# Kernel tuning notes

Measured on AMD Instinct MI355X. Metric: run time of the kernel, lower is better.

## Reference

```python
import jax, jax.numpy as jnp
import numpy as np

VOCAB, EMBED, NFEAT, T, HIDDEN, NCLASS, BATCH = 50000, 50, 3, 120, 300, 5, 1024
D_IN = NFEAT * EMBED  # 150


def setup_inputs() -> dict:
    key = jax.random.key(0)
    ks = jax.random.split(key, 5)
    s_in = 1.0 / np.sqrt(D_IN)
    s_h = 1.0 / np.sqrt(HIDDEN)
    return {
        "ids": jax.random.randint(ks[0], (BATCH, T, NFEAT), 0, VOCAB, dtype=jnp.int32),
        "embed": jax.random.normal(ks[1], (VOCAB, EMBED), dtype=jnp.float32),
        "Wx": jax.random.normal(ks[2], (D_IN, 4 * HIDDEN), dtype=jnp.float32) * s_in,
        "Wh": jax.random.normal(ks[3], (HIDDEN, 4 * HIDDEN), dtype=jnp.float32) * s_h,
        "b": jnp.zeros((4 * HIDDEN,), dtype=jnp.float32),
        "U": jax.random.normal(ks[4], (HIDDEN, NCLASS), dtype=jnp.float32) * s_h,
        "b2": jnp.zeros((NCLASS,), dtype=jnp.float32),
    }


def reference(ids, embed, Wx, Wh, b, U, b2):
    # Embedding lookup + concat windows: (B, T, 3) -> (B, T, 150)
    x = embed[ids].reshape(ids.shape[0], T, D_IN)
    # Precompute input contribution for all timesteps: (B, T, 4H)
    xz = jnp.einsum("btd,dg->btg", x, Wx) + b
    xz = jnp.transpose(xz, (1, 0, 2))  # (T, B, 4H)

    def step(carry, xz_t):
        c, h = carry
        z = xz_t + h @ Wh  # (B, 4H)
        i, f, g, o = jnp.split(z, 4, axis=-1)
        i = jax.nn.sigmoid(i)
        f = jax.nn.sigmoid(f)
        o = jax.nn.sigmoid(o)
        g = jnp.tanh(g)
        c = f * c + i * g
        h = o * jnp.tanh(c)
        # dropout at inference (keep_prob=1) is identity
        y = h @ U + b2  # (B, C)
        return (c, h), y

    B = ids.shape[0]
    init = (jnp.zeros((B, HIDDEN), x.dtype), jnp.zeros((B, HIDDEN), x.dtype))
    _, ys = jax.lax.scan(step, init, xz)  # ys: (T, B, C)
    return jnp.transpose(ys, (1, 0, 2))  # (B, T, C)
```

## Files before the change

### kernel.cpp

```cpp
#include <hip/hip_runtime.h>


#define BATCH 1024
#define TT    120
#define HID   300
#define KX    160
#define KH    320
#define SL    64
#define HSL   60
#define NCOL  1280
#define GH    5
#define GB    32
#define BS    32
#define XST   168
#define FSTR  32
#define NSLOT 3
#define NB    256

typedef __attribute__((ext_vector_type(8))) short bf16x8;
typedef __attribute__((ext_vector_type(4))) float f32x4;

__device__ __forceinline__ unsigned short f2b(float f) {
  union { float f; unsigned u; } v; v.f = f;
  unsigned r = v.u + 0x7fffu + ((v.u >> 16) & 1u);
  return (unsigned short)(r >> 16);
}
__device__ __forceinline__ float sigm(float x) {
  return __builtin_amdgcn_rcpf(1.f + __expf(-x));
}
__device__ __forceinline__ float tanhf_(float x) {
  return 2.f * __builtin_amdgcn_rcpf(1.f + __expf(-2.f * x)) - 1.f;
}

__global__ void k_reorder_wh(const float* __restrict__ W, unsigned short* __restrict__ Wp) {
  int tid = blockIdx.x * 256 + threadIdx.x;
  if (tid >= KH * NCOL) return;
  int c = tid % NCOL, k = tid / NCOL;
  int js = k >> 6, v0 = k & 63;
  int j = c >> 8, r = c & 255, g = r >> 6, u0 = r & 63;
  float val = 0.f;
  if (v0 < HSL && u0 < HSL) val = W[(js * HSL + v0) * 1200 + g * 300 + j * HSL + u0];
  Wp[((k >> 3) * NCOL + c) * 8 + (k & 7)] = f2b(val);
}

__global__ void k_reorder_wx(const float* __restrict__ W, unsigned short* __restrict__ Wp) {
  int tid = blockIdx.x * 256 + threadIdx.x;
  if (tid >= KX * NCOL) return;
  int c = tid % NCOL, k = tid / NCOL;
  int j = c >> 8, r = c & 255, g = r >> 6, u0 = r & 63;
  float val = 0.f;
  if (k < 150 && u0 < HSL) val = W[k * 1200 + g * 300 + j * HSL + u0];
  Wp[((k >> 3) * NCOL + c) * 8 + (k & 7)] = f2b(val);
}

__global__ void k_reorder_b(const float* __restrict__ b, float* __restrict__ bp) {
  int c = blockIdx.x * 256 + threadIdx.x;
  if (c >= NCOL) return;
  int j = c >> 8, r = c & 255, g = r >> 6, u0 = r & 63;
  bp[c] = (u0 < HSL) ? b[g * 300 + j * HSL + u0] : 0.f;
}

__global__ void k_reorder_u(const float* __restrict__ U, unsigned short* __restrict__ Up) {
  int tid = blockIdx.x * 256 + threadIdx.x;
  if (tid >= KH * 16) return;
  int n = tid % 16, k = tid / 16;
  int js = k >> 6, v0 = k & 63;
  float v = (v0 < HSL && n < 5) ? U[(js * HSL + v0) * 5 + n] : 0.f;
  Up[((k >> 3) * 16 + n) * 8 + (k & 7)] = f2b(v);
}

__launch_bounds__(256, 1)
__global__ void k_lstm(const int* __restrict__ ids, const float* __restrict__ embed,
                       const unsigned short* __restrict__ Wp,
                       const unsigned short* __restrict__ Wxp,
                       const float* __restrict__ bp,
                       const unsigned short* __restrict__ Up,
                       unsigned short* __restrict__ hbuf,
                       int* __restrict__ flags,
                       int* __restrict__ xcd_cnt,
                       const float* __restrict__ b2,
                       float* __restrict__ out) {
  __shared__ __align__(16) unsigned short x_lds[2][BS * XST];
  __shared__ char lds_pad[61440];
  __shared__ int role[2];

  const int tid = threadIdx.x;
  if (tid == 0) {
    ((volatile char*)lds_pad)[0] = 0;
    int xcd = __builtin_amdgcn_s_getreg(63508) & 7;
    int rank = atomicAdd(&xcd_cnt[xcd], 1);
    role[0] = xcd; role[1] = rank;
  }
  __syncthreads();
  const int xcd = role[0], rank = role[1];
  if (rank >= GH * 4) return;
  const int bg = xcd * 4 + rank / GH;
  const int j  = rank % GH;

  const int lane = tid & 63, w = tid >> 6;
  const int l15 = lane & 15, l4 = lane >> 4;

  if (tid < BS) {
#pragma unroll
    for (int bq = 0; bq < 2; ++bq)
      for (int e = 150; e < XST; ++e) x_lds[bq][tid * XST + e] = 0;
  }

  const int colb = j * 256 + w * 16 + l15;

  bf16x8 bh[10][4], bx[5][4];
#pragma unroll
  for (int kk = 0; kk < 10; ++kk)
#pragma unroll
    for (int g = 0; g < 4; ++g)
      bh[kk][g] = *(const bf16x8*)(Wp + ((kk * 4 + l4) * NCOL + colb + g * 64) * 8);
#pragma unroll
  for (int kk = 0; kk < 5; ++kk)
#pragma unroll
    for (int g = 0; g < 4; ++g)
      bx[kk][g] = *(const bf16x8*)(Wxp + ((kk * 4 + l4) * NCOL + colb + g * 64) * 8);

  float bias[4];
#pragma unroll
  for (int g = 0; g < 4; ++g) bias[g] = bp[colb + g * 64];
  const float b2v = (l15 < 5) ? b2[l15] : 0.f;

  if (tid < 192) {
    int xrow = tid / 6, half = tid % 6, f = half >> 1, hh = half & 1;
    int nf2 = hh ? 12 : 13;
    int koff = f * 50 + (hh ? 26 : 0);
    int id = ids[((bg * BS + xrow) * TT + 0) * 3 + f];
    const float* src = embed + (long)id * 50 + (hh ? 26 : 0);
    unsigned short* dst = &x_lds[0][xrow * XST + koff];
#pragma unroll
    for (int e = 0; e < 13; ++e)
      if (e < nf2) {
        float2 v = *(const float2*)(src + 2 * e);
        *(unsigned*)(dst + 2 * e) = (unsigned)f2b(v.x) | ((unsigned)f2b(v.y) << 16);
      }
  }
  __syncthreads();

  f32x4 acc[4][2];
  float cst[2][4];
#pragma unroll
  for (int g = 0; g < 4; ++g)
#pragma unroll
    for (int mt = 0; mt < 2; ++mt) acc[g][mt] = {0.f, 0.f, 0.f, 0.f};
#pragma unroll
  for (int mt = 0; mt < 2; ++mt)
#pragma unroll
    for (int r = 0; r < 4; ++r) cst[mt][r] = 0.f;

  {
    const unsigned short* xb = &x_lds[0][l15 * XST + l4 * 8];
#pragma unroll
    for (int kk = 0; kk < 5; ++kk) {
      bf16x8 a0 = *(const bf16x8*)(xb + kk * 32);
      bf16x8 a1 = *(const bf16x8*)(xb + 16 * XST + kk * 32);
#pragma unroll
      for (int g = 0; g < 4; ++g) {
        acc[g][0] = __builtin_amdgcn_mfma_f32_16x16x32_bf16(a0, bx[kk][g], acc[g][0], 0, 0, 0);
        acc[g][1] = __builtin_amdgcn_mfma_f32_16x16x32_bf16(a1, bx[kk][g], acc[g][1], 0, 0, 0);
      }
    }
  }

  bf16x8 va0[10], va1[10];

  for (int t = 0; t < TT; ++t) {
    float2 xv[13];
    int xrow = 0, koff = 0, nf2 = 0;
    const bool xact = (t + 1 < TT) && (tid < 192);
    if (xact) {
      xrow = tid / 6; int half = tid % 6, f = half >> 1, hh = half & 1;
      nf2 = hh ? 12 : 13;
      koff = f * 50 + (hh ? 26 : 0);
      int id = ids[((bg * BS + xrow) * TT + (t + 1)) * 3 + f];
      const float* src = embed + (long)id * 50 + (hh ? 26 : 0);
#pragma unroll
      for (int e = 0; e < 13; ++e)
        if (e < nf2) xv[e] = *(const float2*)(src + 2 * e);
    }

    if (t > 0) {
      if (tid == 0) {
        int* fp = flags + ((t - 1) * GB + bg) * FSTR;
        int it = 0;
        while (__hip_atomic_load(fp, __ATOMIC_RELAXED, __HIP_MEMORY_SCOPE_AGENT) < GH) {
          __builtin_amdgcn_s_sleep(1);
          if (++it > 200000) break;
        }
      }
      __syncthreads();
      asm volatile("buffer_inv\n\ts_waitcnt vmcnt(0)" ::: "memory");

      const unsigned short* ar =
          hbuf + ((t - 1) % NSLOT) * (BATCH * KH) + (bg * BS + l15) * KH + l4 * 8;
#pragma unroll
      for (int kk = 0; kk < 10; ++kk) {
        va0[kk] = *(const bf16x8*)(ar + kk * 32);
        va1[kk] = *(const bf16x8*)(ar + 16 * KH + kk * 32);
      }

#pragma unroll
      for (int kk = 0; kk < 10; ++kk) {
#pragma unroll
        for (int g = 0; g < 4; ++g) {
          acc[g][0] = __builtin_amdgcn_mfma_f32_16x16x32_bf16(va0[kk], bh[kk][g], acc[g][0], 0, 0, 0);
          acc[g][1] = __builtin_amdgcn_mfma_f32_16x16x32_bf16(va1[kk], bh[kk][g], acc[g][1], 0, 0, 0);
        }
      }
    }

    unsigned short* hdst = hbuf + (t % NSLOT) * (BATCH * KH);
#pragma unroll
    for (int mt = 0; mt < 2; ++mt) {
#pragma unroll
      for (int r = 0; r < 4; ++r) {
        float zi = acc[0][mt][r] + bias[0];
        float zf = acc[1][mt][r] + bias[1];
        float zg = acc[2][mt][r] + bias[2];
        float zo = acc[3][mt][r] + bias[3];
        float gi = sigm(zi), gf = sigm(zf), go = sigm(zo), gg = tanhf_(zg);
        float c = gf * cst[mt][r] + gi * gg;
        cst[mt][r] = c;
        float h = go * tanhf_(c);
        unsigned v = f2b(h);
        unsigned p1 = v | ((unsigned)__shfl_xor((int)v, 1) << 16);
        unsigned long long p2 = (unsigned long long)p1 |
            ((unsigned long long)(unsigned)__shfl_xor((int)p1, 2) << 32);
        if ((l15 & 3) == 0) {
          int row = bg * BS + mt * 16 + l4 * 4 + r;
          *(unsigned long long*)(hdst + row * KH + j * SL + w * 16 + l15) = p2;
        }
      }
      acc[0][mt] = {0.f, 0.f, 0.f, 0.f};
      acc[1][mt] = {0.f, 0.f, 0.f, 0.f};
      acc[2][mt] = {0.f, 0.f, 0.f, 0.f};
      acc[3][mt] = {0.f, 0.f, 0.f, 0.f};
    }

    asm volatile("s_waitcnt vmcnt(0)" ::: "memory");
    __syncthreads();
    if (tid == 0)
      __hip_atomic_fetch_add(flags + (t * GB + bg) * FSTR, 1, __ATOMIC_RELAXED,
                             __HIP_MEMORY_SCOPE_AGENT);

    if (t > 0 && j == (t - 1) % GH && w == 0) {
      f32x4 ay0 = {0.f, 0.f, 0.f, 0.f}, ay1 = {0.f, 0.f, 0.f, 0.f};
#pragma unroll
      for (int kk = 0; kk < 10; ++kk) {
        bf16x8 u = *(const bf16x8*)(Up + ((kk * 4 + l4) * 16 + l15) * 8);
        ay0 = __builtin_amdgcn_mfma_f32_16x16x32_bf16(va0[kk], u, ay0, 0, 0, 0);
        ay1 = __builtin_amdgcn_mfma_f32_16x16x32_bf16(va1[kk], u, ay1, 0, 0, 0);
      }
      if (l15 < 5) {
#pragma unroll
        for (int q = 0; q < 4; ++q) {
          out[((bg * BS + l4 * 4 + q) * TT + (t - 1)) * 5 + l15] = ay0[q] + b2v;
          out[((bg * BS + 16 + l4 * 4 + q) * TT + (t - 1)) * 5 + l15] = ay1[q] + b2v;
        }
      }
    }

    if (xact) {
      unsigned short* dst = &x_lds[(t + 1) & 1][xrow * XST + koff];
#pragma unroll
      for (int e = 0; e < 13; ++e)
        if (e < nf2)
          *(unsigned*)(dst + 2 * e) = (unsigned)f2b(xv[e].x) | ((unsigned)f2b(xv[e].y) << 16);
    }
    __syncthreads();

    if (t + 1 < TT) {
      const unsigned short* xb = &x_lds[(t + 1) & 1][l15 * XST + l4 * 8];
#pragma unroll
      for (int kk = 0; kk < 5; ++kk) {
        bf16x8 a0 = *(const bf16x8*)(xb + kk * 32);
        bf16x8 a1 = *(const bf16x8*)(xb + 16 * XST + kk * 32);
#pragma unroll
        for (int g = 0; g < 4; ++g) {
          acc[g][0] = __builtin_amdgcn_mfma_f32_16x16x32_bf16(a0, bx[kk][g], acc[g][0], 0, 0, 0);
          acc[g][1] = __builtin_amdgcn_mfma_f32_16x16x32_bf16(a1, bx[kk][g], acc[g][1], 0, 0, 0);
        }
      }
    }
  }

  if (j == (TT - 1) % GH) {
    if (tid == 0) {
      int* fp = flags + ((TT - 1) * GB + bg) * FSTR;
      int it = 0;
      while (__hip_atomic_load(fp, __ATOMIC_RELAXED, __HIP_MEMORY_SCOPE_AGENT) < GH) {
        __builtin_amdgcn_s_sleep(1);
        if (++it > 200000) break;
      }
    }
    __syncthreads();
    asm volatile("buffer_inv\n\ts_waitcnt vmcnt(0)" ::: "memory");
    const unsigned short* ar =
        hbuf + ((TT - 1) % NSLOT) * (BATCH * KH) + (bg * BS + l15) * KH + l4 * 8;
#pragma unroll
    for (int kk = 0; kk < 10; ++kk) {
      va0[kk] = *(const bf16x8*)(ar + kk * 32);
      va1[kk] = *(const bf16x8*)(ar + 16 * KH + kk * 32);
    }
    if (w == 0) {
      f32x4 ay0 = {0.f, 0.f, 0.f, 0.f}, ay1 = {0.f, 0.f, 0.f, 0.f};
#pragma unroll
      for (int kk = 0; kk < 10; ++kk) {
        bf16x8 u = *(const bf16x8*)(Up + ((kk * 4 + l4) * 16 + l15) * 8);
        ay0 = __builtin_amdgcn_mfma_f32_16x16x32_bf16(va0[kk], u, ay0, 0, 0, 0);
        ay1 = __builtin_amdgcn_mfma_f32_16x16x32_bf16(va1[kk], u, ay1, 0, 0, 0);
      }
      if (l15 < 5) {
#pragma unroll
        for (int q = 0; q < 4; ++q) {
          out[((bg * BS + l4 * 4 + q) * TT + (TT - 1)) * 5 + l15] = ay0[q] + b2v;
          out[((bg * BS + 16 + l4 * 4 + q) * TT + (TT - 1)) * 5 + l15] = ay1[q] + b2v;
        }
      }
    }
  }
}

extern "C" void kernel_launch(void* const* d_in, const int* in_sizes, int n_in,
                              void* d_out, int out_size, void* d_ws, size_t ws_size,
                              hipStream_t stream) {
  const int*   ids   = (const int*)d_in[0];
  const float* embed = (const float*)d_in[1];
  const float* Wx    = (const float*)d_in[2];
  const float* Wh    = (const float*)d_in[3];
  const float* b     = (const float*)d_in[4];
  const float* U     = (const float*)d_in[5];
  const float* b2    = (const float*)d_in[6];
  float* out = (float*)d_out;

  char* ws = (char*)d_ws;
  size_t off = 0;
  unsigned short* Wp   = (unsigned short*)(ws + off); off += (size_t)KH * NCOL * 2;
  unsigned short* Wxp  = (unsigned short*)(ws + off); off += (size_t)KX * NCOL * 2;
  float*          bp   = (float*)(ws + off);          off += (size_t)NCOL * 4;
  unsigned short* Up   = (unsigned short*)(ws + off); off += (size_t)KH * 16 * 2;
  unsigned short* hbuf = (unsigned short*)(ws + off); off += (size_t)NSLOT * BATCH * KH * 2;
  int*            flags= (int*)(ws + off);            off += (size_t)TT * GB * FSTR * 4;
  int*            xcd_cnt = (int*)(ws + off);         off += 8 * 4;
  if (ws_size < off) return;

  hipMemsetAsync(flags, 0, TT * GB * FSTR * 4 + 8 * 4, stream);
  k_reorder_wh<<<(KH * NCOL + 255) / 256, 256, 0, stream>>>(Wh, Wp);
  k_reorder_wx<<<(KX * NCOL + 255) / 256, 256, 0, stream>>>(Wx, Wxp);
  k_reorder_b<<<(NCOL + 255) / 256, 256, 0, stream>>>(b, bp);
  k_reorder_u<<<(KH * 16 + 255) / 256, 256, 0, stream>>>(U, Up);

  k_lstm<<<dim3(NB), dim3(256), 0, stream>>>(ids, embed, Wp, Wxp, bp, Up,
                                             hbuf, flags, xcd_cnt, b2, out);
}
```

Before: 717.5 us.

## Use per-wave flag sync, deeper embedding prefetch, split output projection across waves

Replaces the block-level spin-wait plus __syncthreads with every wave polling the inter-block flag directly, and has each wave signal completion itself (threshold becomes GH*4 arrivals). This removes two block barriers per timestep. The embedding gather is software-pipelined two steps ahead, with ids prefetched three steps ahead, and the output projection is split across waves 2 and 3 instead of serialized on wave 0. The trade-offs are more global atomic polling traffic, a longer sleep-free busy spin, and more live registers for the prefetched embeddings.

```diff
diff --git a/kernel.cpp b/kernel.cpp
--- a/kernel.cpp
+++ b/kernel.cpp
@@ -16,6 +16,7 @@
 #define FSTR  32
 #define NSLOT 3
 #define NB    256
+#define NREL  (GH * 4)
 
 typedef __attribute__((ext_vector_type(8))) short bf16x8;
 typedef __attribute__((ext_vector_type(4))) float f32x4;
@@ -70,6 +71,7 @@
 }
 
 __launch_bounds__(256, 1)
+__attribute__((amdgpu_waves_per_eu(1, 1)))
 __global__ void k_lstm(const int* __restrict__ ids, const float* __restrict__ embed,
                        const unsigned short* __restrict__ Wp,
                        const unsigned short* __restrict__ Wxp,
@@ -125,12 +127,19 @@
   for (int g = 0; g < 4; ++g) bias[g] = bp[colb + g * 64];
   const float b2v = (l15 < 5) ? b2[l15] : 0.f;
 
-  if (tid < 192) {
-    int xrow = tid / 6, half = tid % 6, f = half >> 1, hh = half & 1;
-    int nf2 = hh ? 12 : 13;
-    int koff = f * 50 + (hh ? 26 : 0);
-    int id = ids[((bg * BS + xrow) * TT + 0) * 3 + f];
-    const float* src = embed + (long)id * 50 + (hh ? 26 : 0);
+  int xrow = 0, koff = 0, nf2 = 0, f = 0;
+  const bool gth = (tid < 192);
+  if (gth) {
+    xrow = tid / 6; int half = tid % 6; f = half >> 1; int hh = half & 1;
+    nf2 = hh ? 12 : 13;
+    koff = f * 50 + (hh ? 26 : 0);
+  }
+  const long idbase = (long)(bg * BS + xrow) * TT * 3 + f;
+  const int  eoff   = (koff - f * 50);
+
+  if (gth) {
+    int id0 = ids[idbase + 0 * 3];
+    const float* src = embed + (long)id0 * 50 + eoff;
     unsigned short* dst = &x_lds[0][xrow * XST + koff];
 #pragma unroll
     for (int e = 0; e < 13; ++e)
@@ -166,33 +175,26 @@
     }
   }
 
+  float2 xv[13];
+  int idv = 0;
+  if (gth) {
+    int id1 = ids[idbase + 1 * 3];
+    const float* src = embed + (long)id1 * 50 + eoff;
+#pragma unroll
+    for (int e = 0; e < 13; ++e)
+      if (e < nf2) xv[e] = *(const float2*)(src + 2 * e);
+    idv = ids[idbase + 2 * 3];
+  }
+
   bf16x8 va0[10], va1[10];
 
   for (int t = 0; t < TT; ++t) {
-    float2 xv[13];
-    int xrow = 0, koff = 0, nf2 = 0;
-    const bool xact = (t + 1 < TT) && (tid < 192);
-    if (xact) {
-      xrow = tid / 6; int half = tid % 6, f = half >> 1, hh = half & 1;
-      nf2 = hh ? 12 : 13;
-      koff = f * 50 + (hh ? 26 : 0);
-      int id = ids[((bg * BS + xrow) * TT + (t + 1)) * 3 + f];
-      const float* src = embed + (long)id * 50 + (hh ? 26 : 0);
-#pragma unroll
-      for (int e = 0; e < 13; ++e)
-        if (e < nf2) xv[e] = *(const float2*)(src + 2 * e);
-    }
-
     if (t > 0) {
-      if (tid == 0) {
-        int* fp = flags + ((t - 1) * GB + bg) * FSTR;
-        int it = 0;
-        while (__hip_atomic_load(fp, __ATOMIC_RELAXED, __HIP_MEMORY_SCOPE_AGENT) < GH) {
-          __builtin_amdgcn_s_sleep(1);
-          if (++it > 200000) break;
-        }
-      }
-      __syncthreads();
+      const int* fp = flags + ((t - 1) * GB + bg) * FSTR;
+      int it = 0;
+      while (__hip_atomic_load(fp, __ATOMIC_RELAXED, __HIP_MEMORY_SCOPE_AGENT) < NREL) {
+        if (++it > 300000) break;
+      }
       asm volatile("buffer_inv\n\ts_waitcnt vmcnt(0)" ::: "memory");
 
       const unsigned short* ar =
@@ -202,7 +204,6 @@
         va0[kk] = *(const bf16x8*)(ar + kk * 32);
         va1[kk] = *(const bf16x8*)(ar + 16 * KH + kk * 32);
       }
-
 #pragma unroll
       for (int kk = 0; kk < 10; ++kk) {
 #pragma unroll
@@ -242,38 +243,45 @@
     }
 
     asm volatile("s_waitcnt vmcnt(0)" ::: "memory");
-    __syncthreads();
-    if (tid == 0)
+    if ((tid & 63) == 0)
       __hip_atomic_fetch_add(flags + (t * GB + bg) * FSTR, 1, __ATOMIC_RELAXED,
                              __HIP_MEMORY_SCOPE_AGENT);
 
-    if (t > 0 && j == (t - 1) % GH && w == 0) {
-      f32x4 ay0 = {0.f, 0.f, 0.f, 0.f}, ay1 = {0.f, 0.f, 0.f, 0.f};
-#pragma unroll
-      for (int kk = 0; kk < 10; ++kk) {
-        bf16x8 u = *(const bf16x8*)(Up + ((kk * 4 + l4) * 16 + l15) * 8);
-        ay0 = __builtin_amdgcn_mfma_f32_16x16x32_bf16(va0[kk], u, ay0, 0, 0, 0);
-        ay1 = __builtin_amdgcn_mfma_f32_16x16x32_bf16(va1[kk], u, ay1, 0, 0, 0);
-      }
-      if (l15 < 5) {
-#pragma unroll
-        for (int q = 0; q < 4; ++q) {
-          out[((bg * BS + l4 * 4 + q) * TT + (t - 1)) * 5 + l15] = ay0[q] + b2v;
-          out[((bg * BS + 16 + l4 * 4 + q) * TT + (t - 1)) * 5 + l15] = ay1[q] + b2v;
-        }
-      }
-    }
-
-    if (xact) {
-      unsigned short* dst = &x_lds[(t + 1) & 1][xrow * XST + koff];
-#pragma unroll
-      for (int e = 0; e < 13; ++e)
-        if (e < nf2)
-          *(unsigned*)(dst + 2 * e) = (unsigned)f2b(xv[e].x) | ((unsigned)f2b(xv[e].y) << 16);
-    }
-    __syncthreads();
+    if (t > 0 && j == (t - 1) % GH) {
+      if (w == 2) {
+        f32x4 ay = {0.f, 0.f, 0.f, 0.f};
+#pragma unroll
+        for (int kk = 0; kk < 10; ++kk) {
+          bf16x8 u = *(const bf16x8*)(Up + ((kk * 4 + l4) * 16 + l15) * 8);
+          ay = __builtin_amdgcn_mfma_f32_16x16x32_bf16(va0[kk], u, ay, 0, 0, 0);
+        }
+        if (l15 < 5)
+#pragma unroll
+          for (int q = 0; q < 4; ++q)
+            out[((bg * BS + l4 * 4 + q) * TT + (t - 1)) * 5 + l15] = ay[q] + b2v;
+      } else if (w == 3) {
+        f32x4 ay = {0.f, 0.f, 0.f, 0.f};
+#pragma unroll
+        for (int kk = 0; kk < 10; ++kk) {
+          bf16x8 u = *(const bf16x8*)(Up + ((kk * 4 + l4) * 16 + l15) * 8);
+          ay = __builtin_amdgcn_mfma_f32_16x16x32_bf16(va1[kk], u, ay, 0, 0, 0);
+        }
+        if (l15 < 5)
+#pragma unroll
+          for (int q = 0; q < 4; ++q)
+            out[((bg * BS + 16 + l4 * 4 + q) * TT + (t - 1)) * 5 + l15] = ay[q] + b2v;
+      }
+    }
 
     if (t + 1 < TT) {
+      if (gth) {
+        unsigned short* dst = &x_lds[(t + 1) & 1][xrow * XST + koff];
+#pragma unroll
+        for (int e = 0; e < 13; ++e)
+          if (e < nf2)
+            *(unsigned*)(dst + 2 * e) = (unsigned)f2b(xv[e].x) | ((unsigned)f2b(xv[e].y) << 16);
+      }
+      __syncthreads();
       const unsigned short* xb = &x_lds[(t + 1) & 1][l15 * XST + l4 * 8];
 #pragma unroll
       for (int kk = 0; kk < 5; ++kk) {
@@ -285,19 +293,22 @@
           acc[g][1] = __builtin_amdgcn_mfma_f32_16x16x32_bf16(a1, bx[kk][g], acc[g][1], 0, 0, 0);
         }
       }
+      if (gth && t + 2 < TT) {
+        const float* src = embed + (long)idv * 50 + eoff;
+#pragma unroll
+        for (int e = 0; e < 13; ++e)
+          if (e < nf2) xv[e] = *(const float2*)(src + 2 * e);
+        if (t + 3 < TT) idv = ids[idbase + (long)(t + 3) * 3];
+      }
     }
   }
 
   if (j == (TT - 1) % GH) {
-    if (tid == 0) {
-      int* fp = flags + ((TT - 1) * GB + bg) * FSTR;
-      int it = 0;
-      while (__hip_atomic_load(fp, __ATOMIC_RELAXED, __HIP_MEMORY_SCOPE_AGENT) < GH) {
-        __builtin_amdgcn_s_sleep(1);
-        if (++it > 200000) break;
-      }
-    }
-    __syncthreads();
+    const int* fp = flags + ((TT - 1) * GB + bg) * FSTR;
+    int it = 0;
+    while (__hip_atomic_load(fp, __ATOMIC_RELAXED, __HIP_MEMORY_SCOPE_AGENT) < NREL) {
+      if (++it > 300000) break;
+    }
     asm volatile("buffer_inv\n\ts_waitcnt vmcnt(0)" ::: "memory");
     const unsigned short* ar =
         hbuf + ((TT - 1) % NSLOT) * (BATCH * KH) + (bg * BS + l15) * KH + l4 * 8;
@@ -306,21 +317,28 @@
       va0[kk] = *(const bf16x8*)(ar + kk * 32);
       va1[kk] = *(const bf16x8*)(ar + 16 * KH + kk * 32);
     }
-    if (w == 0) {
-      f32x4 ay0 = {0.f, 0.f, 0.f, 0.f}, ay1 = {0.f, 0.f, 0.f, 0.f};
+    if (w == 2) {
+      f32x4 ay = {0.f, 0.f, 0.f, 0.f};
 #pragma unroll
       for (int kk = 0; kk < 10; ++kk) {
         bf16x8 u = *(const bf16x8*)(Up + ((kk * 4 + l4) * 16 + l15) * 8);
-        ay0 = __builtin_amdgcn_mfma_f32_16x16x32_bf16(va0[kk], u, ay0, 0, 0, 0);
-        ay1 = __builtin_amdgcn_mfma_f32_16x16x32_bf16(va1[kk], u, ay1, 0, 0, 0);
-      }
-      if (l15 < 5) {
-#pragma unroll
-        for (int q = 0; q < 4; ++q) {
-          out[((bg * BS + l4 * 4 + q) * TT + (TT - 1)) * 5 + l15] = ay0[q] + b2v;
-          out[((bg * BS + 16 + l4 * 4 + q) * TT + (TT - 1)) * 5 + l15] = ay1[q] + b2v;
-        }
-      }
+        ay = __builtin_amdgcn_mfma_f32_16x16x32_bf16(va0[kk], u, ay, 0, 0, 0);
+      }
+      if (l15 < 5)
+#pragma unroll
+        for (int q = 0; q < 4; ++q)
+          out[((bg * BS + l4 * 4 + q) * TT + (TT - 1)) * 5 + l15] = ay[q] + b2v;
+    } else if (w == 3) {
+      f32x4 ay = {0.f, 0.f, 0.f, 0.f};
+#pragma unroll
+      for (int kk = 0; kk < 10; ++kk) {
+        bf16x8 u = *(const bf16x8*)(Up + ((kk * 4 + l4) * 16 + l15) * 8);
+        ay = __builtin_amdgcn_mfma_f32_16x16x32_bf16(va1[kk], u, ay, 0, 0, 0);
+      }
+      if (l15 < 5)
+#pragma unroll
+        for (int q = 0; q < 4; ++q)
+          out[((bg * BS + 16 + l4 * 4 + q) * TT + (TT - 1)) * 5 + l15] = ay[q] + b2v;
     }
   }
 }
```

Result: no change. 711.8 us (-0.8%).
